# Kernel optimization log

Measured on AMD Instinct MI355X. Metric: run time of the kernel, lower is better.

## Reference

```python
import jax, jax.numpy as jnp
import numpy as np
from jax.scipy.special import logsumexp

B, T, LD, HD, K = 64, 2048, 16, 64, 8
TEMP = 1.0  # annealing=False
LOG2PI = float(np.log(2.0 * np.pi))


def setup_inputs() -> dict:
    key = jax.random.key(0)
    ks = jax.random.split(key, 10)
    return {
        "z": jax.random.normal(ks[0], (B, T, LD), jnp.float32),
        "pi": jax.random.normal(ks[1], (K,), jnp.float32) * 0.5,
        "Q": jax.random.normal(ks[2], (K, K), jnp.float32) * 0.5,
        "init_mean": jax.random.normal(ks[3], (K, LD), jnp.float32),
        # torch init: rand(K,1,1) * eye(LD) * 5  (a scale factor per state)
        "init_cov": jax.random.uniform(ks[4], (K, 1, 1), jnp.float32) * 5.0 * jnp.eye(LD, dtype=jnp.float32)[None],
        "covs": jnp.tile(jnp.eye(LD, dtype=jnp.float32)[None], (K, 1, 1)) + 0.05 * jax.random.normal(ks[5], (K, LD, LD), jnp.float32),
        "W1": jax.random.normal(ks[6], (K, HD, LD), jnp.float32) / np.sqrt(LD),
        "b1": jnp.zeros((K, HD), jnp.float32),
        "W2": jax.random.normal(ks[7], (K, LD, HD), jnp.float32) / np.sqrt(HD),
        "b2": jnp.zeros((K, LD), jnp.float32),
    }


def _chol_terms(C):
    """Sigma = C C^T + 1e-6 I ; return (L^{-1}, 0.5*logdet) per state."""
    dim = C.shape[-1]
    Sigma = C @ jnp.swapaxes(C, -1, -2) + 1e-6 * jnp.eye(dim, dtype=C.dtype)
    L = jnp.linalg.cholesky(Sigma)  # [K,D,D]
    Linv = jax.vmap(lambda l: jax.scipy.linalg.solve_triangular(l, jnp.eye(dim, dtype=C.dtype), lower=True))(L)
    logdet_half = jnp.sum(jnp.log(jnp.diagonal(L, axis1=-2, axis2=-1)), -1)  # [K]
    return Linv, logdet_half


def _mvn_logp(diff, Linv, logdet_half):
    # diff [B,t,K,D], Linv [K,D,D] -> [B,t,K]
    y = jnp.einsum('kde,btke->btkd', Linv, diff)
    maha = jnp.sum(y * y, -1)
    d = diff.shape[-1]
    return -0.5 * maha - logdet_half - 0.5 * d * LOG2PI


def reference(z, pi, Q, init_mean, init_cov, covs, W1, b1, W2, b2):
    # ---- local evidence: log p(z_1|s_1), log p(z_t | z_{t-1}, s_t)  [B,T,K]
    Linv0, ld0 = _chol_terms(init_cov)
    le1 = _mvn_logp(z[:, :1, None, :] - init_mean, Linv0, ld0)  # [B,1,K]
    zp = z[:, :-1]  # [B,T-1,D]
    h = jax.nn.softplus(jnp.einsum('btd,khd->btkh', zp, W1) + b1)  # per-state MLP hidden
    mu = jnp.einsum('btkh,kdh->btkd', h, W2) + b2  # [B,T-1,K,D]
    LinvT, ldT = _chol_terms(covs)
    leT = _mvn_logp(z[:, 1:, None, :] - mu, LinvT, ldT)  # [B,T-1,K]
    le = jnp.concatenate([le1, leT], axis=1)  # [B,T,K]

    # ---- alpha recursion (filtering)
    logpi = jax.nn.log_softmax(pi / TEMP)
    Qlog = jax.nn.log_softmax(Q / TEMP, axis=-1)  # log p(s_t=j | s_{t-1}=i)
    QT = Qlog.T  # [to, from]
    lp0 = le[:, 0] + logpi
    lz0 = logsumexp(lp0, -1)
    la0 = lp0 - lz0[:, None]
    le_rest = jnp.swapaxes(le[:, 1:], 0, 1)  # [T-1,B,K]

    def astep(la_prev, le_t):
        lp = logsumexp(le_t[:, :, None] + QT[None] + la_prev[:, None, :], axis=-1)
        lz = logsumexp(lp, -1)
        la = lp - lz[:, None]
        return la, (la, lz)

    _, (las, lzs) = jax.lax.scan(astep, la0, le_rest)
    log_alpha = jnp.concatenate([la0[:, None], jnp.swapaxes(las, 0, 1)], axis=1)  # [B,T,K]
    log_Z = jnp.concatenate([lz0[:, None], lzs.T], axis=1)  # [B,T]

    # ---- beta recursion (smoothing), reverse scan
    def bstep(lb_next, inp):
        le_t, lz_t = inp
        lb = logsumexp(Qlog[None] + le_t[:, None, :] + lb_next[:, None, :], axis=-1) - lz_t[:, None]
        return lb, lb

    _, lbs = jax.lax.scan(bstep, jnp.zeros((B, K), le.dtype), (le_rest, log_Z[:, 1:].T), reverse=True)
    log_beta = jnp.concatenate([jnp.swapaxes(lbs, 0, 1), jnp.zeros((B, 1, K), le.dtype)], axis=1)

    # ---- posteriors
    gamma = jnp.exp(log_alpha + log_beta)  # [B,T,K]
    paired = jnp.exp(Qlog[None, None] + log_alpha[:, :-1, :, None] + log_beta[:, 1:, None, :] + le[:, 1:, None, :] - log_Z[:, 1:, None, None])  # [B,T-1,K,K]
    return gamma, paired, log_Z
```

## Files before the change

### kernel.cpp

```cpp
#include <hip/hip_runtime.h>

#define B_ 64
#define T_ 2048
#define LD_ 16
#define HD_ 64
#define K_ 8
#define L_ 16
#define C_ 128
#define S_ 16

constexpr int OFF_LE    = 0;
constexpr int OFF_ALPHA = 1048576;
constexpr int OFF_EBAR  = 2097152;
constexpr int OFF_ZT    = OFF_ALPHA;
constexpr int OFF_PBUF  = 3145728;
constexpr int OFF_RLOG  = 3670016;
constexpr int OFF_SBUF  = 3809280;
constexpr int OFF_UBUF  = 3874816;
constexpr int OFF_ULOG  = 3940352;
constexpr int OFF_SAIN  = 3941376;
constexpr int OFF_BENT  = 3949568;
constexpr int OFF_PRM   = 3957760;

constexpr int P_LINV0 = 0;
constexpr int P_LINVT = 2048;
constexpr int P_LD0   = 4096;
constexpr int P_LDT   = 4104;
constexpr int P_LOGPI = 4112;
constexpr int P_QEXP  = 4120;
constexpr int P_QTEXP = 4184;

constexpr int FI_NC2 = 32768;
constexpr int FI_C0I = 32896;

constexpr int OUT_PAIRED = B_*T_*K_;
constexpr int OUT_LOGZ   = OUT_PAIRED + B_*(T_-1)*K_*K_;

template<int CTRL>
__device__ __forceinline__ float dppmov(float x) {
  int xi = __float_as_int(x);
  int r = __builtin_amdgcn_update_dpp(xi, xi, CTRL, 0xF, 0xF, true);
  return __int_as_float(r);
}
__device__ __forceinline__ void allg8(float v, float w[8]) {
  w[0] = v;
  w[1] = dppmov<0xB1>(v);
  w[2] = dppmov<0x4E>(v);
  w[3] = dppmov<0x4E>(w[1]);
  w[7] = dppmov<0x141>(v);
  w[6] = dppmov<0xB1>(w[7]);
  w[5] = dppmov<0x4E>(w[7]);
  w[4] = dppmov<0x4E>(w[6]);
}
template<int V> __device__ __forceinline__ float xorg8(float x);
template<> __device__ __forceinline__ float xorg8<0>(float x) { return x; }
template<> __device__ __forceinline__ float xorg8<1>(float x) { return dppmov<0xB1>(x); }
template<> __device__ __forceinline__ float xorg8<2>(float x) { return dppmov<0x4E>(x); }
template<> __device__ __forceinline__ float xorg8<3>(float x) { return dppmov<0x4E>(dppmov<0xB1>(x)); }
template<> __device__ __forceinline__ float xorg8<4>(float x) { return dppmov<0x4E>(dppmov<0xB1>(dppmov<0x141>(x))); }
template<> __device__ __forceinline__ float xorg8<5>(float x) { return dppmov<0x4E>(dppmov<0x141>(x)); }
template<> __device__ __forceinline__ float xorg8<6>(float x) { return dppmov<0xB1>(dppmov<0x141>(x)); }
template<> __device__ __forceinline__ float xorg8<7>(float x) { return dppmov<0x141>(x); }

__device__ __forceinline__ float bfly_sum8(float x) {
  x += dppmov<0xB1>(x); x += dppmov<0x4E>(x); x += dppmov<0x141>(x); return x;
}
__device__ __forceinline__ float bfly_max8(float x) {
  x = fmaxf(x, dppmov<0xB1>(x)); x = fmaxf(x, dppmov<0x4E>(x)); x = fmaxf(x, dppmov<0x141>(x)); return x;
}
__device__ __forceinline__ float rcpnr(float x) {
  float r0 = __builtin_amdgcn_rcpf(x);
  return r0 * __builtin_fmaf(-x, r0, 2.0f);
}
__device__ __forceinline__ void absg8(float v, float w[8]) {
  int x = __float_as_int(v);
  w[0] = __int_as_float(__builtin_amdgcn_ds_swizzle(x, 0x18));
  w[1] = __int_as_float(__builtin_amdgcn_ds_swizzle(x, 0x38));
  w[2] = __int_as_float(__builtin_amdgcn_ds_swizzle(x, 0x58));
  w[3] = __int_as_float(__builtin_amdgcn_ds_swizzle(x, 0x78));
  w[4] = __int_as_float(__builtin_amdgcn_ds_swizzle(x, 0x98));
  w[5] = __int_as_float(__builtin_amdgcn_ds_swizzle(x, 0xB8));
  w[6] = __int_as_float(__builtin_amdgcn_ds_swizzle(x, 0xD8));
  w[7] = __int_as_float(__builtin_amdgcn_ds_swizzle(x, 0xF8));
}
__device__ __forceinline__ void col2row(const float cl[8], float rv[8]) {
  rv[0] = cl[0];
  rv[1] = xorg8<1>(cl[1]);
  rv[2] = xorg8<2>(cl[2]);
  rv[3] = xorg8<3>(cl[3]);
  rv[4] = xorg8<4>(cl[4]);
  rv[5] = xorg8<5>(cl[5]);
  rv[6] = xorg8<6>(cl[6]);
  rv[7] = xorg8<7>(cl[7]);
}
__device__ __forceinline__ void mmul8(const float a[8], const float m[8], float o[8]) {
  float m8[8][8];
  #pragma unroll
  for (int w = 0; w < 8; w++) allg8(m[w], m8[w]);
  #pragma unroll
  for (int v = 0; v < 8; v++) {
    float acc = 0.f;
    #pragma unroll
    for (int u = 0; u < 8; u++) acc = __builtin_fmaf(a[u], m8[u^v][u], acc);
    o[v] = acc;
  }
}
__device__ __forceinline__ float maxnorm8(float m[8]) {
  float mx = m[0];
  #pragma unroll
  for (int u = 1; u < 8; u++) mx = fmaxf(mx, m[u]);
  mx = bfly_max8(mx);
  float r = rcpnr(mx);
  #pragma unroll
  for (int u = 0; u < 8; u++) m[u] *= r;
  return mx;
}
__device__ __forceinline__ void load_rows(const float* p, float r[8]) {
  const float4* q = (const float4*)p;
  float4 x0 = q[0], x1 = q[1];
  r[0]=x0.x; r[1]=x0.y; r[2]=x0.z; r[3]=x0.w;
  r[4]=x1.x; r[5]=x1.y; r[6]=x1.z; r[7]=x1.w;
}
__device__ __forceinline__ float dotw8(const float r[8], const float w[8]) {
  return ((r[0]*w[0]+r[1]*w[1]) + (r[2]*w[2]+r[3]*w[3]))
       + ((r[4]*w[4]+r[5]*w[5]) + (r[6]*w[6]+r[7]*w[7]));
}

typedef __attribute__((ext_vector_type(4))) float f32x4;
typedef __attribute__((ext_vector_type(8))) short bf16x8;

__device__ __forceinline__ unsigned ph(float a, float b) {
  return (__float_as_uint(a) >> 16) | (__float_as_uint(b) & 0xFFFF0000u);
}
__device__ __forceinline__ float hif(float a) {
  return __uint_as_float(__float_as_uint(a) & 0xFFFF0000u);
}
__device__ __forceinline__ bf16x8 u2f(uint4 u) {
  return __builtin_bit_cast(bf16x8, u);
}
__device__ __forceinline__ uint4 mkfrag_u4(float4 v) {
  unsigned ux = __float_as_uint(v.x), uy = __float_as_uint(v.y);
  unsigned uz = __float_as_uint(v.z), uw = __float_as_uint(v.w);
  unsigned h01 = (ux >> 16) | (uy & 0xFFFF0000u);
  unsigned h23 = (uz >> 16) | (uw & 0xFFFF0000u);
  float lx = v.x - __uint_as_float(ux & 0xFFFF0000u);
  float ly = v.y - __uint_as_float(uy & 0xFFFF0000u);
  float lz = v.z - __uint_as_float(uz & 0xFFFF0000u);
  float lw = v.w - __uint_as_float(uw & 0xFFFF0000u);
  unsigned l01 = ph(lx, ly);
  unsigned l23 = ph(lz, lw);
  return make_uint4(h01, h23, l01, l23);
}
__device__ __forceinline__ f32x4 MF(bf16x8 a, bf16x8 b, f32x4 c) {
  return __builtin_amdgcn_mfma_f32_16x16x32_bf16(a, b, c, 0, 0, 0);
}

__global__ __launch_bounds__(64) void prep_kernel(
    const float* __restrict__ pi, const float* __restrict__ Q,
    const float* __restrict__ init_cov, const float* __restrict__ covs,
    float* __restrict__ prm)
{
  int tid = threadIdx.x;
  int blk = blockIdx.x;
  if (blk < 16) {
    int k = blk & 7;
    const float* C = (blk < 8 ? init_cov : covs) + k*256;
    float* outL  = prm + (blk < 8 ? P_LINV0 : P_LINVT) + k*256;
    float* outld = prm + (blk < 8 ? P_LD0   : P_LDT)   + k;
    __shared__ float S[16][17], L[16][17], X[16][17];
    for (int e = tid; e < 256; e += 64) {
      int r = e >> 4, c = e & 15;
      float s = (r == c) ? 1e-6f : 0.f;
      for (int l = 0; l < 16; l++) s += C[r*16+l] * C[c*16+l];
      S[r][c] = s;
    }
    __syncthreads();
    for (int j = 0; j < 16; j++) {
      if (tid == 0) L[j][j] = sqrtf(S[j][j]);
      __syncthreads();
      if (tid > j && tid < 16) L[tid][j] = S[tid][j] / L[j][j];
      __syncthreads();
      if (tid > j && tid < 16) {
        float ltj = L[tid][j];
        for (int c = j+1; c <= tid; c++) S[tid][c] -= ltj * L[c][j];
      }
      __syncthreads();
    }
    if (tid < 16) {
      int c = tid;
      for (int r = 0; r < 16; r++) {
        float v;
        if (r < c) v = 0.f;
        else {
          v = (r == c) ? 1.f : 0.f;
          for (int s2 = c; s2 < r; s2++) v -= L[r][s2] * X[s2][c];
          v /= L[r][r];
        }
        X[r][c] = v;
      }
    }
    __syncthreads();
    for (int e = tid; e < 256; e += 64) outL[e] = X[e>>4][e&15];
    if (tid == 0) {
      float ld = 0.f;
      for (int j = 0; j < 16; j++) ld += logf(L[j][j]);
      *outld = ld;
    }
  } else {
    if (tid < 8) {
      int row = tid;
      float q[8], mx = -1e30f;
      for (int j = 0; j < 8; j++) { q[j] = Q[row*8+j]; mx = fmaxf(mx, q[j]); }
      float s = 0.f;
      for (int j = 0; j < 8; j++) s += __expf(q[j]-mx);
      float ls = logf(s);
      for (int j = 0; j < 8; j++) {
        float e = __expf(q[j]-mx-ls);
        prm[P_QEXP  + row*8 + j] = e;
        prm[P_QTEXP + j*8 + row] = e;
      }
    } else if (tid == 8) {
      float p[8], mx = -1e30f;
      for (int j = 0; j < 8; j++) { p[j] = pi[j]; mx = fmaxf(mx, p[j]); }
      float s = 0.f;
      for (int j = 0; j < 8; j++) s += __expf(p[j]-mx);
      float ls = logf(s);
      for (int j = 0; j < 8; j++) prm[P_LOGPI+j] = p[j]-mx-ls;
    }
  }
}

__global__ __launch_bounds__(64) void prep2_kernel(
    const float* __restrict__ W1, const float* __restrict__ W2,
    const float* __restrict__ b2, const float* __restrict__ init_mean,
    const float* __restrict__ prm, float* __restrict__ frag)
{
  int k = blockIdx.x, tid = threadIdx.x;
  __shared__ float Ls[16][16], L0s[16][16], G[16][64];
  for (int e = tid; e < 256; e += 64) {
    Ls[e>>4][e&15]  = prm[P_LINVT + k*256 + e];
    L0s[e>>4][e&15] = prm[P_LINV0 + k*256 + e];
  }
  __syncthreads();
  for (int idx = tid; idx < 1024; idx += 64) {
    int d = idx >> 6, hh = idx & 63;
    float s = 0.f;
    for (int e = 0; e < 16; e++) s += Ls[d][e] * W2[k*1024 + e*64 + hh];
    G[d][hh] = -s;
  }
  __syncthreads();
  int d = tid & 15, q = tid >> 4;
  uint4* F4 = (uint4*)frag;
  for (int kc = 0; kc < 2; kc++) {
    float v[8], lo[8];
    for (int j = 0; j < 8; j++) {
      int hh = 32*kc + 16*(j>>2) + 4*q + (j&3);
      v[j] = G[d][hh];
      lo[j] = v[j] - hif(v[j]);
    }
    F4[6144 + ((k*2+kc)*4+q)*16 + d] =
        make_uint4(ph(v[0],v[1]), ph(v[2],v[3]), ph(v[4],v[5]), ph(v[6],v[7]));
    F4[7168 + ((k*2+kc)*4+q)*16 + d] =
        make_uint4(ph(lo[0],lo[1]), ph(lo[2],lo[3]), ph(lo[4],lo[5]), ph(lo[6],lo[7]));
  }
  for (int mt = 0; mt < 4; mt++) {
    int hh = 16*mt + d;
    float v[4], lo[4];
    for (int j = 0; j < 4; j++) { v[j] = W1[k*1024 + hh*16 + 4*q + j]; lo[j] = v[j] - hif(v[j]); }
    unsigned x = ph(v[0],v[1]), y = ph(v[2],v[3]);
    F4[((k*4+mt)*4+q)*16 + d]        = make_uint4(x, y, x, y);
    F4[2048 + ((k*4+mt)*4+q)*16 + d] = make_uint4(ph(lo[0],lo[1]), ph(lo[2],lo[3]), 0u, 0u);
  }
  {
    float v[4], lo[4];
    for (int j = 0; j < 4; j++) { v[j] = Ls[d][4*q+j]; lo[j] = v[j] - hif(v[j]); }
    unsigned x = ph(v[0],v[1]), y = ph(v[2],v[3]);
    F4[4096 + (k*4+q)*16 + d] = make_uint4(x, y, x, y);
    F4[4608 + (k*4+q)*16 + d] = make_uint4(ph(lo[0],lo[1]), ph(lo[2],lo[3]), 0u, 0u);
    for (int j = 0; j < 4; j++) { v[j] = L0s[d][4*q+j]; lo[j] = v[j] - hif(v[j]); }
    x = ph(v[0],v[1]); y = ph(v[2],v[3]);
    F4[5120 + (k*4+q)*16 + d] = make_uint4(x, y, x, y);
    F4[5632 + (k*4+q)*16 + d] = make_uint4(ph(lo[0],lo[1]), ph(lo[2],lo[3]), 0u, 0u);
  }
  if (q == 0) {
    float s2 = 0.f, s0 = 0.f;
    for (int e = 0; e < 16; e++) {
      s2 += Ls[d][e]  * b2[k*16+e];
      s0 += L0s[d][e] * init_mean[k*16+e];
    }
    frag[FI_NC2 + k*16 + d] = -s2;
    frag[FI_C0I + k*16 + d] = -s0;
  }
}

__global__ __launch_bounds__(256) void ztr_kernel(
    const float* __restrict__ z, uint4* __restrict__ zf)
{
  int tid = blockIdx.x*256 + threadIdx.x;
  int t = tid >> 6, b = tid & 63;
  const float4* src = (const float4*)(z + (b*T_ + t)*LD_);
  #pragma unroll
  for (int q = 0; q < 4; q++)
    zf[(t*4 + q)*64 + b] = mkfrag_u4(src[q]);
}

__global__ __launch_bounds__(256) void emisB_kernel(
    const uint4* __restrict__ zf, const float* __restrict__ b1,
    const float* __restrict__ frag, const float* __restrict__ prm,
    float* __restrict__ lebuf)
{
  int lane = threadIdx.x & 63;
  int wid = __builtin_amdgcn_readfirstlane(blockIdx.x*4 + (threadIdx.x >> 6));
  int bblk = wid & 3;
  int tch  = (wid >> 2) & 255;
  int k    = wid >> 10;
  int c = lane & 15, q = lane >> 4;
  int b = bblk*16 + c;
  const uint4* F4 = (const uint4*)frag;

  bf16x8 w1a1[4], w1a2[4];
  #pragma unroll
  for (int mt = 0; mt < 4; mt++) {
    w1a1[mt] = u2f(F4[((k*4+mt)*4+q)*16 + c]);
    w1a2[mt] = u2f(F4[2048 + ((k*4+mt)*4+q)*16 + c]);
  }
  bf16x8 lva1 = u2f(F4[4096 + (k*4+q)*16 + c]);
  bf16x8 lva2 = u2f(F4[4608 + (k*4+q)*16 + c]);
  bf16x8 gahi[2], galo[2];
  #pragma unroll
  for (int kc = 0; kc < 2; kc++) {
    gahi[kc] = u2f(F4[6144 + ((k*2+kc)*4+q)*16 + c]);
    galo[kc] = u2f(F4[7168 + ((k*2+kc)*4+q)*16 + c]);
  }
  float b1iv[16];
  #pragma unroll
  for (int i = 0; i < 16; i++)
    b1iv[i] = b1[k*64 + (i>>2)*16 + 4*q + (i&3)];
  float nc2[4];
  #pragma unroll
  for (int r = 0; r < 4; r++) nc2[r] = frag[FI_NC2 + k*16 + 4*q + r];
  float lconst = -prm[P_LDT + k] - 14.70301653f;

  int t0 = tch*8;
  bf16x8 zp;
  int ttstart;
  if (tch == 0) {
    bf16x8 zc0 = u2f(zf[q*64 + b]);
    bf16x8 l0a1 = u2f(F4[5120 + (k*4+q)*16 + c]);
    bf16x8 l0a2 = u2f(F4[5632 + (k*4+q)*16 + c]);
    f32x4 acc;
    acc[0] = frag[FI_C0I + k*16 + 4*q + 0];
    acc[1] = frag[FI_C0I + k*16 + 4*q + 1];
    acc[2] = frag[FI_C0I + k*16 + 4*q + 2];
    acc[3] = frag[FI_C0I + k*16 + 4*q + 3];
    acc = MF(l0a1, zc0, acc);
    acc = MF(l0a2, zc0, acc);
    float m2 = (acc[0]*acc[0] + acc[1]*acc[1]) + (acc[2]*acc[2] + acc[3]*acc[3]);
    m2 += __shfl_xor(m2, 16);
    m2 += __shfl_xor(m2, 32);
    float le = -0.5f*m2 - prm[P_LD0+k] - 14.70301653f + prm[P_LOGPI+k];
    if (q == 0) lebuf[k*64 + b] = le;
    zp = zc0;
    ttstart = 1;
  } else {
    zp = u2f(zf[((t0-1)*4 + q)*64 + b]);
    ttstart = 0;
  }

  uint4 zvu = zf[((t0+ttstart)*4 + q)*64 + b];
  #pragma unroll 1
  for (int tt = ttstart; tt < 8; tt++) {
    int t = t0 + tt;
    uint4 zvn = zvu;
    if (tt < 7) zvn = zf[((t+1)*4 + q)*64 + b];
    bf16x8 zc = u2f(zvu);
    f32x4 a1[4];
    #pragma unroll
    for (int mt = 0; mt < 4; mt++) {
      f32x4 ai;
      ai[0] = b1iv[mt*4+0]; ai[1] = b1iv[mt*4+1];
      ai[2] = b1iv[mt*4+2]; ai[3] = b1iv[mt*4+3];
      ai = MF(w1a1[mt], zp, ai);
      a1[mt] = MF(w1a2[mt], zp, ai);
    }
    float hv[16];
    #pragma unroll
    for (int i = 0; i < 16; i++) {
      float a = a1[i>>2][i&3];
      hv[i] = __logf(1.f + __expf(a));
    }
    bf16x8 hhi[2], hlo[2];
    #pragma unroll
    for (int kc = 0; kc < 2; kc++) {
      const float* hp = hv + 8*kc;
      hhi[kc] = u2f(make_uint4(ph(hp[0],hp[1]), ph(hp[2],hp[3]),
                               ph(hp[4],hp[5]), ph(hp[6],hp[7])));
      float l0 = hp[0]-hif(hp[0]), l1 = hp[1]-hif(hp[1]);
      float l2 = hp[2]-hif(hp[2]), l3 = hp[3]-hif(hp[3]);
      float l4 = hp[4]-hif(hp[4]), l5 = hp[5]-hif(hp[5]);
      float l6 = hp[6]-hif(hp[6]), l7 = hp[7]-hif(hp[7]);
      hlo[kc] = u2f(make_uint4(ph(l0,l1), ph(l2,l3), ph(l4,l5), ph(l6,l7)));
    }
    f32x4 acc;
    acc[0] = nc2[0]; acc[1] = nc2[1]; acc[2] = nc2[2]; acc[3] = nc2[3];
    acc = MF(lva1, zc, acc);
    acc = MF(lva2, zc, acc);
    #pragma unroll
    for (int kc = 0; kc < 2; kc++) {
      acc = MF(gahi[kc], hhi[kc], acc);
      acc = MF(galo[kc], hhi[kc], acc);
      acc = MF(gahi[kc], hlo[kc], acc);
    }
    float m2 = (acc[0]*acc[0] + acc[1]*acc[1]) + (acc[2]*acc[2] + acc[3]*acc[3]);
    m2 += __shfl_xor(m2, 16);
    m2 += __shfl_xor(m2, 32);
    float le = -0.5f*m2 + lconst;
    if (q == 0) lebuf[t*512 + k*64 + b] = le;
    zp = zc;
    zvu = zvn;
  }
}

__global__ __launch_bounds__(256) void fwdA_kernel(
    const float* __restrict__ lebuf, const float* __restrict__ prm,
    float* __restrict__ pbuf, float* __restrict__ sbuf)
{
  int lane64 = threadIdx.x & 63;
  int iu = threadIdx.x >> 6;
  int unit = blockIdx.x*4 + iu;
  int b = unit & 63, s = unit >> 6;
  int u = lane64 >> 3, j = lane64 & 7;
  int c = 8*s + u;
  float qtv[64];
  #pragma unroll
  for (int x = 0; x < 8; x++)
    #pragma unroll
    for (int v = 0; v < 8; v++)
      qtv[x*8+v] = prm[P_QTEXP + (j^x)*8 + (j^v)];
  float lev[16];
  #pragma unroll
  for (int x = 0; x < 16; x++) lev[x] = lebuf[(c*L_+x)*512 + j*64 + b];
  float pl[8];
  if (c == 0) {
    float m = bfly_max8(lev[0]);
    float e = __expf(lev[0]-m);
    allg8(e, pl);
  } else {
    float m = bfly_max8(lev[0]);
    float e = __expf(lev[0]-m);
    float e8[8]; allg8(e, e8);
    float np[8];
    #pragma unroll
    for (int x = 0; x < 8; x++) np[x] = e8[x] * qtv[x*8];
    float mx = np[0];
    #pragma unroll
    for (int x = 1; x < 8; x++) mx = fmaxf(mx, np[x]);
    mx = bfly_max8(mx);
    float r = rcpnr(mx);
    #pragma unroll
    for (int x = 0; x < 8; x++) pl[x] = np[x] * r;
  }
  #pragma unroll
  for (int sx = 1; sx < 16; sx++) {
    float m = bfly_max8(lev[sx]);
    float e = __expf(lev[sx]-m);
    float e8[8]; allg8(e, e8);
    float np[8];
    #pragma unroll
    for (int x = 0; x < 8; x++) {
      float acc = 0.f;
      #pragma unroll
      for (int v = 0; v < 8; v++) acc = __builtin_fmaf(qtv[x*8+v], pl[v], acc);
      np[x] = e8[x] * acc;
    }
    float mx = np[0];
    #pragma unroll
    for (int x = 1; x < 8; x++) mx = fmaxf(mx, np[x]);
    mx = bfly_max8(mx);
    float r = rcpnr(mx);
    #pragma unroll
    for (int x = 0; x < 8; x++) pl[x] = np[x] * r;
  }
  float rv[8]; col2row(pl, rv);
  float4* dst = (float4*)(pbuf + (c*64 + b)*64 + j*8);
  dst[0] = make_float4(rv[0], rv[1], rv[2], rv[3]);
  dst[1] = make_float4(rv[4], rv[5], rv[6], rv[7]);
  __shared__ float M[4][8][64];
  #pragma unroll
  for (int v = 0; v < 8; v++) M[iu][u][j*8+v] = rv[v];
  __syncthreads();
  if (u == 0) {
    float m[8];
    #pragma unroll
    for (int v = 0; v < 8; v++) m[v] = M[iu][0][j*8+v];
    for (int cc = 1; cc < 8; cc++) {
      float a[8];
      #pragma unroll
      for (int v = 0; v < 8; v++) a[v] = M[iu][cc][j*8+v];
      float nm[8];
      mmul8(a, m, nm);
      maxnorm8(nm);
      #pragma unroll
      for (int v = 0; v < 8; v++) m[v] = nm[v];
    }
    float4* d2 = (float4*)(sbuf + (s*64 + b)*64 + j*8);
    d2[0] = make_float4(m[0], m[1], m[2], m[3]);
    d2[1] = make_float4(m[4], m[5], m[6], m[7]);
  }
}

__global__ __launch_bounds__(512) void fwdP2b_kernel(
    const float* __restrict__ sbuf, float* __restrict__ sain)
{
  int lane = threadIdx.x;
  int b = lane >> 3, i = lane & 7;
  const float4* base = (const float4*)sbuf;
  float4 c0 = base[(0*64+b)*16 + i*2], c1 = base[(0*64+b)*16 + i*2 + 1];
  float a = 0.125f;
  for (int s = 0; s < 16; s++) {
    int s2 = (s < 15) ? s+1 : 15;
    float4 n0 = base[(s2*64+b)*16 + i*2], n1 = base[(s2*64+b)*16 + i*2 + 1];
    float aw[8]; allg8(a, aw);
    float sm = ((c0.x*aw[0] + c0.y*aw[1]) + (c0.z*aw[2] + c0.w*aw[3]))
             + ((c1.x*aw[4] + c1.y*aw[5]) + (c1.z*aw[6] + c1.w*aw[7]));
    float tot = bfly_sum8(sm);
    float an = sm * rcpnr(tot);
    if (s < 15) { a = an; sain[(s+1)*512 + b*8 + i] = a; }
    c0 = n0; c1 = n1;
  }
}

__global__ __launch_bounds__(256) void fwdB_kernel(
    const float* __restrict__ lebuf, const float* __restrict__ prm,
    const float* __restrict__ sain, float* pbuf,
    float* __restrict__ alpha, float* __restrict__ ebar,
    float* __restrict__ rlog, float* __restrict__ ubuf,
    float* __restrict__ ulog, float* __restrict__ out)
{
  int lane64 = threadIdx.x & 63;
  int iu = threadIdx.x >> 6;
  int unit = blockIdx.x*4 + iu;
  int b = unit & 63, s = unit >> 6;
  int u = lane64 >> 3, i = lane64 & 7;
  int c = 8*s + u;
  int off = b*8 + i;
  __shared__ float Als[4][8];
  __shared__ float Mh[4][8][64];
  __shared__ float Lh[4][8];
  float pr[8];
  load_rows(pbuf + (c*64 + b)*64 + i*8, pr);
  float lev[16];
  #pragma unroll
  for (int x = 0; x < 16; x++) lev[x] = lebuf[(c*L_+x)*512 + i*64 + b];
  float av_in = 0.f;
  if (u == 0) av_in = (s == 0) ? 0.125f : sain[s*512 + off];
  for (int r = 0; r < 7; r++) {
    if (u == r) {
      if (r > 0) av_in = Als[iu][i];
      float aw[8]; allg8(av_in, aw);
      float sm = dotw8(pr, aw);
      float tot = bfly_sum8(sm);
      Als[iu][i] = sm * rcpnr(tot);
    }
    __syncthreads();
  }
  if (u == 7) av_in = Als[iu][i];
  float q[8];
  #pragma unroll
  for (int x = 0; x < 8; x++) q[x] = prm[P_QTEXP + i*8 + (i^x)];
  float* logZ = out + OUT_LOGZ + b*T_;
  float eb_loc[16];
  float a;
  if (c == 0) {
    float m0 = bfly_max8(lev[0]);
    float e0x = __expf(lev[0]-m0);
    float ct = bfly_sum8(e0x);
    float rr = rcpnr(ct);
    a = e0x * rr;
    alpha[off] = a;
    eb_loc[0] = a;
    ebar[off] = a;
    if (i == 0) logZ[0] = m0 + __logf(ct);
  } else {
    a = av_in;
    int t = c*L_;
    float m = bfly_max8(lev[0]);
    float e = __expf(lev[0]-m);
    float w[8]; allg8(a, w);
    float dot = dotw8(q, w);
    float p = e * dot;
    float ct = bfly_sum8(p);
    float rr = rcpnr(ct);
    a = p * rr;
    alpha[t*512 + off] = a;
    float eb = e * rr;
    eb_loc[0] = eb;
    ebar[t*512 + off] = eb;
    if (i == 0) logZ[t] = m + __logf(ct);
  }
  #pragma unroll
  for (int x = 1; x < 16; x++) {
    int t = c*L_ + x;
    float m = bfly_max8(lev[x]);
    float e = __expf(lev[x]-m);
    float w[8]; allg8(a, w);
    float dot = dotw8(q, w);
    float p = e * dot;
    float ct = bfly_sum8(p);
    float rr = rcpnr(ct);
    a = p * rr;
    alpha[t*512 + off] = a;
    float eb = e * rr;
    eb_loc[x] = eb;
    ebar[t*512 + off] = eb;
    if (i == 0) logZ[t] = m + __logf(ct);
  }
  float qv[64];
  #pragma unroll
  for (int x = 0; x < 8; x++)
    #pragma unroll
    for (int v = 0; v < 8; v++)
      qv[x*8+v] = prm[P_QEXP + (i^x)*8 + (i^v)];
  float rl8[8];
  #pragma unroll
  for (int x = 0; x < 8; x++) rl8[x] = (x == 0) ? 1.f : 0.f;
  float lsc = 0.f;
  #pragma unroll
  for (int sx = 15; sx >= 1; sx--) {
    float e8[8]; allg8(eb_loc[sx], e8);
    float nr[8];
    #pragma unroll
    for (int x = 0; x < 8; x++) {
      float acc = 0.f;
      #pragma unroll
      for (int v = 0; v < 8; v++) acc = __builtin_fmaf(qv[x*8+v], e8[v]*rl8[v], acc);
      nr[x] = acc;
    }
    float mx = nr[0];
    #pragma unroll
    for (int x = 1; x < 8; x++) mx = fmaxf(mx, nr[x]);
    mx = bfly_max8(mx);
    float r = rcpnr(mx);
    #pragma unroll
    for (int x = 0; x < 8; x++) rl8[x] = nr[x] * r;
    lsc += __logf(mx);
  }
  float rv[8]; col2row(rl8, rv);
  float4* dstR = (float4*)(pbuf + (c*64 + b)*64 + i*8);
  dstR[0] = make_float4(rv[0], rv[1], rv[2], rv[3]);
  dstR[1] = make_float4(rv[4], rv[5], rv[6], rv[7]);
  if (i == 0) rlog[c*64 + b] = lsc;
  float qr[8];
  #pragma unroll
  for (int x = 0; x < 8; x++) qr[x] = prm[P_QEXP + i*8 + (i^x)];
  float d8[8];
  #pragma unroll
  for (int v = 0; v < 8; v++) d8[v] = eb_loc[0] * rv[v];
  float h8[8];
  mmul8(qr, d8, h8);
  float ls = lsc + __logf(maxnorm8(h8));
  #pragma unroll
  for (int v = 0; v < 8; v++) Mh[iu][u][i*8+v] = h8[v];
  if (i == 0) Lh[iu][u] = ls;
  __syncthreads();
  if (u == 0) {
    float m[8];
    #pragma unroll
    for (int v = 0; v < 8; v++) m[v] = Mh[iu][7][i*8+v];
    float lsum = Lh[iu][7];
    for (int cc = 6; cc >= 0; cc--) {
      float aa[8];
      #pragma unroll
      for (int v = 0; v < 8; v++) aa[v] = Mh[iu][cc][i*8+v];
      float t8[8];
      mmul8(aa, m, t8);
      lsum += Lh[iu][cc] + __logf(maxnorm8(t8));
      #pragma unroll
      for (int v = 0; v < 8; v++) m[v] = t8[v];
    }
    float4* d2 = (float4*)(ubuf + (s*64 + b)*64 + i*8);
    d2[0] = make_float4(m[0], m[1], m[2], m[3]);
    d2[1] = make_float4(m[4], m[5], m[6], m[7]);
    if (i == 0) ulog[s*64 + b] = lsum;
  }
}

__global__ __launch_bounds__(512) void bwdP2b_kernel(
    const float* __restrict__ ubuf, const float* __restrict__ ulog,
    float* __restrict__ bent)
{
  int lane = threadIdx.x;
  int b = lane >> 3, i = lane & 7;
  bent[15*512 + b*8 + i] = 1.f;
  const float4* base = (const float4*)ubuf;
  float sh = 1.f, sig = 0.f;
  float4 c0 = base[(15*64+b)*16 + i*2], c1 = base[(15*64+b)*16 + i*2 + 1];
  float cu = ulog[15*64 + b];
  for (int s = 15; s >= 1; s--) {
    int s2 = (s > 1) ? s-1 : 1;
    float4 n0 = base[(s2*64+b)*16 + i*2], n1 = base[(s2*64+b)*16 + i*2 + 1];
    float nu = ulog[s2*64 + b];
    float sw[8]; allg8(sh, sw);
    float y = ((c0.x*sw[0] + c0.y*sw[1]) + (c0.z*sw[2] + c0.w*sw[3]))
            + ((c1.x*sw[4] + c1.y*sw[5]) + (c1.z*sw[6] + c1.w*sw[7]));
    float mx = bfly_max8(y);
    sh = y * rcpnr(mx);
    sig += cu + __logf(mx);
    bent[(s-1)*512 + b*8 + i] = sh * __expf(sig);
    c0 = n0; c1 = n1; cu = nu;
  }
}

__global__ __launch_bounds__(256) void bwdC_kernel(
    const float* __restrict__ alpha, const float* __restrict__ ebar,
    const float* __restrict__ rbuf, const float* __restrict__ rlog,
    const float* __restrict__ prm, const float* __restrict__ bent,
    float* __restrict__ out)
{
  int lane64 = threadIdx.x & 63;
  int iu = threadIdx.x >> 6;
  int unit = blockIdx.x*4 + iu;
  int b = unit & 63, s = unit >> 6;
  int u = lane64 >> 3, i = lane64 & 7;
  int c = 8*s + u;
  int off = b*8 + i;
  float qr[8], qa[8];
  #pragma unroll
  for (int x = 0; x < 8; x++) qr[x] = prm[P_QEXP + i*8 + (i^x)];
  #pragma unroll
  for (int v = 0; v < 8; v++) qa[v] = prm[P_QEXP + i*8 + v];
  float r8[8];
  load_rows(rbuf + (c*64 + b)*64 + i*8, r8);
  float e0 = ebar[(c*L_)*512 + off];
  float erl = __expf(rlog[c*64 + b]);
  float av[16], ev[16];
  #pragma unroll
  for (int x = 0; x < 16; x++) av[x] = alpha[(c*L_+x)*512 + off];
  #pragma unroll
  for (int x = 1; x < 16; x++) ev[x] = ebar[(c*L_+x)*512 + off];
  float avm1 = (c > 0) ? alpha[(c*L_-1)*512 + off] : 0.f;
  __shared__ float Bls[4][8];
  float bt = 0.f, y = 0.f, nbv = 0.f;
  for (int r = 7; r >= 0; r--) {
    if (u == r) {
      bt = (r == 7) ? bent[s*512 + off] : Bls[iu][i];
      float bw[8]; allg8(bt, bw);
      y = dotw8(r8, bw) * erl;
      float ey = e0 * y;
      float w[8]; allg8(ey, w);
      nbv = 0.f;
      #pragma unroll
      for (int v = 0; v < 8; v++) nbv = __builtin_fmaf(qr[v], w[v], nbv);
      if (r > 0) Bls[iu][i] = nbv;
    }
    __syncthreads();
  }
  float* po = out + OUT_PAIRED + b*((T_-1)*64);
  float* go = out + b*(T_*K_);
  float bb = bt;
  if (c == 127) go[2047*8 + i] = av[15];
  #pragma unroll
  for (int x = 15; x >= 1; x--) {
    float eya[8]; absg8(ev[x]*bb, eya);
    float term[8];
    #pragma unroll
    for (int v = 0; v < 8; v++) term[v] = qa[v]*eya[v];
    float nb = ((term[0]+term[1]) + (term[2]+term[3]))
             + ((term[4]+term[5]) + (term[6]+term[7]));
    int t = c*L_ + x - 1;
    float am = av[x-1];
    float4* pd = (float4*)(po + t*64 + i*8);
    pd[0] = make_float4(am*term[0], am*term[1], am*term[2], am*term[3]);
    pd[1] = make_float4(am*term[4], am*term[5], am*term[6], am*term[7]);
    go[t*8 + i] = am*nb;
    bb = nb;
  }
  if (c > 0) {
    float eya[8]; absg8(e0*y, eya);
    int t = c*L_ - 1;
    float4* pd = (float4*)(po + t*64 + i*8);
    pd[0] = make_float4(avm1*qa[0]*eya[0], avm1*qa[1]*eya[1],
                        avm1*qa[2]*eya[2], avm1*qa[3]*eya[3]);
    pd[1] = make_float4(avm1*qa[4]*eya[4], avm1*qa[5]*eya[5],
                        avm1*qa[6]*eya[6], avm1*qa[7]*eya[7]);
    go[t*8 + i] = avm1 * nbv;
  }
}

extern "C" void kernel_launch(void* const* d_in, const int* in_sizes, int n_in,
                              void* d_out, int out_size, void* d_ws, size_t ws_size,
                              hipStream_t stream) {
  const float* z         = (const float*)d_in[0];
  const float* pi        = (const float*)d_in[1];
  const float* Q         = (const float*)d_in[2];
  const float* init_mean = (const float*)d_in[3];
  const float* init_cov  = (const float*)d_in[4];
  const float* covs      = (const float*)d_in[5];
  const float* W1        = (const float*)d_in[6];
  const float* b1        = (const float*)d_in[7];
  const float* W2        = (const float*)d_in[8];
  const float* b2        = (const float*)d_in[9];
  float* out = (float*)d_out;
  float* ws  = (float*)d_ws;

  prep_kernel<<<17, 64, 0, stream>>>(pi, Q, init_cov, covs, ws + OFF_PRM);
  prep2_kernel<<<8, 64, 0, stream>>>(W1, W2, b2, init_mean, ws + OFF_PRM,
                                     ws + OFF_UBUF);
  ztr_kernel<<<512, 256, 0, stream>>>(z, (uint4*)(ws + OFF_ZT));
  emisB_kernel<<<2048, 256, 0, stream>>>((const uint4*)(ws + OFF_ZT), b1,
                                         ws + OFF_UBUF, ws + OFF_PRM,
                                         ws + OFF_LE);
  fwdA_kernel<<<256, 256, 0, stream>>>(ws + OFF_LE, ws + OFF_PRM,
                                       ws + OFF_PBUF, ws + OFF_SBUF);
  fwdP2b_kernel<<<1, 512, 0, stream>>>(ws + OFF_SBUF, ws + OFF_SAIN);
  fwdB_kernel<<<256, 256, 0, stream>>>(ws + OFF_LE, ws + OFF_PRM, ws + OFF_SAIN,
                                       ws + OFF_PBUF, ws + OFF_ALPHA,
                                       ws + OFF_EBAR, ws + OFF_RLOG,
                                       ws + OFF_UBUF, ws + OFF_ULOG, out);
  bwdP2b_kernel<<<1, 512, 0, stream>>>(ws + OFF_UBUF, ws + OFF_ULOG, ws + OFF_BENT);
  bwdC_kernel<<<256, 256, 0, stream>>>(ws + OFF_ALPHA, ws + OFF_EBAR,
                                       ws + OFF_PBUF, ws + OFF_RLOG,
                                       ws + OFF_PRM, ws + OFF_BENT, out);
}
```

Before: 283.9 us.

## Halve HMM chunk length, drop ebar buffer, compute Q softmax per block

Reduces the per-chunk time length of the chunked forward/backward scan from 16 to 8, doubling the number of chunks and blocks. This shortens the serial work per thread and the register footprint, at the cost of longer sequential cross-chunk passes (32 steps instead of 16). The ebar intermediate is no longer written to global memory. The backward kernel instead recomputes it from the log-evidence and logZ, trading extra exp work for less memory traffic. The softmax of Q is computed in shared memory inside each block rather than read from a precomputed parameter buffer.

Result: faster. 234.1 us (-17.5%).

```diff
diff --git a/kernel.cpp b/kernel.cpp
--- a/kernel.cpp
+++ b/kernel.cpp
@@ -5,30 +5,28 @@
 #define LD_ 16
 #define HD_ 64
 #define K_ 8
-#define L_ 16
-#define C_ 128
-#define S_ 16
+#define L_ 8
+#define C_ 256
+#define S_ 32
 
 constexpr int OFF_LE    = 0;
 constexpr int OFF_ALPHA = 1048576;
-constexpr int OFF_EBAR  = 2097152;
 constexpr int OFF_ZT    = OFF_ALPHA;
-constexpr int OFF_PBUF  = 3145728;
-constexpr int OFF_RLOG  = 3670016;
-constexpr int OFF_SBUF  = 3809280;
-constexpr int OFF_UBUF  = 3874816;
-constexpr int OFF_ULOG  = 3940352;
-constexpr int OFF_SAIN  = 3941376;
-constexpr int OFF_BENT  = 3949568;
-constexpr int OFF_PRM   = 3957760;
+constexpr int OFF_SBUF  = 2097152;
+constexpr int OFF_UBUF  = 2228224;
+constexpr int OFF_RLOG  = 2359296;
+constexpr int OFF_ULOG  = 2375680;
+constexpr int OFF_SAIN  = 2377728;
+constexpr int OFF_BENT  = 2394112;
+constexpr int OFF_PBUF  = 2410496;
+constexpr int OFF_PRML  = 3459072;
+constexpr int OFF_FRAG  = 3463680;
 
 constexpr int P_LINV0 = 0;
 constexpr int P_LINVT = 2048;
 constexpr int P_LD0   = 4096;
 constexpr int P_LDT   = 4104;
 constexpr int P_LOGPI = 4112;
-constexpr int P_QEXP  = 4120;
-constexpr int P_QTEXP = 4184;
 
 constexpr int FI_NC2 = 32768;
 constexpr int FI_C0I = 32896;
@@ -125,6 +123,20 @@
   return ((r[0]*w[0]+r[1]*w[1]) + (r[2]*w[2]+r[3]*w[3]))
        + ((r[4]*w[4]+r[5]*w[5]) + (r[6]*w[6]+r[7]*w[7]));
 }
+__device__ __forceinline__ void fill_Qe(const float* __restrict__ Qm, float* Qe) {
+  if (threadIdx.x < 8) {
+    int r = threadIdx.x;
+    float qq[8], mx = -1e30f;
+    #pragma unroll
+    for (int c2 = 0; c2 < 8; c2++) { qq[c2] = Qm[r*8+c2]; mx = fmaxf(mx, qq[c2]); }
+    float s = 0.f;
+    #pragma unroll
+    for (int c2 = 0; c2 < 8; c2++) s += __expf(qq[c2]-mx);
+    float ls = __logf(s);
+    #pragma unroll
+    for (int c2 = 0; c2 < 8; c2++) Qe[r*8+c2] = __expf(qq[c2]-mx-ls);
+  }
+}
 
 typedef __attribute__((ext_vector_type(4))) float f32x4;
 typedef __attribute__((ext_vector_type(8))) short bf16x8;
@@ -147,9 +159,7 @@
   float ly = v.y - __uint_as_float(uy & 0xFFFF0000u);
   float lz = v.z - __uint_as_float(uz & 0xFFFF0000u);
   float lw = v.w - __uint_as_float(uw & 0xFFFF0000u);
-  unsigned l01 = ph(lx, ly);
-  unsigned l23 = ph(lz, lw);
-  return make_uint4(h01, h23, l01, l23);
+  return make_uint4(h01, h23, ph(lx,ly), ph(lz,lw));
 }
 __device__ __forceinline__ f32x4 MF(bf16x8 a, bf16x8 b, f32x4 c) {
   return __builtin_amdgcn_mfma_f32_16x16x32_bf16(a, b, c, 0, 0, 0);
@@ -207,19 +217,7 @@
       *outld = ld;
     }
   } else {
-    if (tid < 8) {
-      int row = tid;
-      float q[8], mx = -1e30f;
-      for (int j = 0; j < 8; j++) { q[j] = Q[row*8+j]; mx = fmaxf(mx, q[j]); }
-      float s = 0.f;
-      for (int j = 0; j < 8; j++) s += __expf(q[j]-mx);
-      float ls = logf(s);
-      for (int j = 0; j < 8; j++) {
-        float e = __expf(q[j]-mx-ls);
-        prm[P_QEXP  + row*8 + j] = e;
-        prm[P_QTEXP + j*8 + row] = e;
-      }
-    } else if (tid == 8) {
+    if (tid == 0) {
       float p[8], mx = -1e30f;
       for (int j = 0; j < 8; j++) { p[j] = pi[j]; mx = fmaxf(mx, p[j]); }
       float s = 0.f;
@@ -422,24 +420,28 @@
 }
 
 __global__ __launch_bounds__(256) void fwdA_kernel(
-    const float* __restrict__ lebuf, const float* __restrict__ prm,
+    const float* __restrict__ lebuf, const float* __restrict__ Qm,
     float* __restrict__ pbuf, float* __restrict__ sbuf)
 {
+  __shared__ float Qe[64];
+  __shared__ float M[4][8][64];
+  fill_Qe(Qm, Qe);
   int lane64 = threadIdx.x & 63;
   int iu = threadIdx.x >> 6;
   int unit = blockIdx.x*4 + iu;
   int b = unit & 63, s = unit >> 6;
   int u = lane64 >> 3, j = lane64 & 7;
   int c = 8*s + u;
+  float lev[8];
+  #pragma unroll
+  for (int x = 0; x < 8; x++) lev[x] = lebuf[(c*L_+x)*512 + j*64 + b];
+  __syncthreads();
   float qtv[64];
   #pragma unroll
   for (int x = 0; x < 8; x++)
     #pragma unroll
     for (int v = 0; v < 8; v++)
-      qtv[x*8+v] = prm[P_QTEXP + (j^x)*8 + (j^v)];
-  float lev[16];
-  #pragma unroll
-  for (int x = 0; x < 16; x++) lev[x] = lebuf[(c*L_+x)*512 + j*64 + b];
+      qtv[x*8+v] = Qe[(j^v)*8 + (j^x)];
   float pl[8];
   if (c == 0) {
     float m = bfly_max8(lev[0]);
@@ -461,7 +463,7 @@
     for (int x = 0; x < 8; x++) pl[x] = np[x] * r;
   }
   #pragma unroll
-  for (int sx = 1; sx < 16; sx++) {
+  for (int sx = 1; sx < 8; sx++) {
     float m = bfly_max8(lev[sx]);
     float e = __expf(lev[sx]-m);
     float e8[8]; allg8(e, e8);
@@ -485,7 +487,6 @@
   float4* dst = (float4*)(pbuf + (c*64 + b)*64 + j*8);
   dst[0] = make_float4(rv[0], rv[1], rv[2], rv[3]);
   dst[1] = make_float4(rv[4], rv[5], rv[6], rv[7]);
-  __shared__ float M[4][8][64];
   #pragma unroll
   for (int v = 0; v < 8; v++) M[iu][u][j*8+v] = rv[v];
   __syncthreads();
@@ -517,26 +518,31 @@
   const float4* base = (const float4*)sbuf;
   float4 c0 = base[(0*64+b)*16 + i*2], c1 = base[(0*64+b)*16 + i*2 + 1];
   float a = 0.125f;
-  for (int s = 0; s < 16; s++) {
-    int s2 = (s < 15) ? s+1 : 15;
+  for (int s = 0; s < S_; s++) {
+    int s2 = (s < S_-1) ? s+1 : S_-1;
     float4 n0 = base[(s2*64+b)*16 + i*2], n1 = base[(s2*64+b)*16 + i*2 + 1];
     float aw[8]; allg8(a, aw);
     float sm = ((c0.x*aw[0] + c0.y*aw[1]) + (c0.z*aw[2] + c0.w*aw[3]))
              + ((c1.x*aw[4] + c1.y*aw[5]) + (c1.z*aw[6] + c1.w*aw[7]));
     float tot = bfly_sum8(sm);
     float an = sm * rcpnr(tot);
-    if (s < 15) { a = an; sain[(s+1)*512 + b*8 + i] = a; }
+    if (s < S_-1) { a = an; sain[(s+1)*512 + b*8 + i] = a; }
     c0 = n0; c1 = n1;
   }
 }
 
 __global__ __launch_bounds__(256) void fwdB_kernel(
-    const float* __restrict__ lebuf, const float* __restrict__ prm,
+    const float* __restrict__ lebuf, const float* __restrict__ Qm,
     const float* __restrict__ sain, float* pbuf,
-    float* __restrict__ alpha, float* __restrict__ ebar,
-    float* __restrict__ rlog, float* __restrict__ ubuf,
-    float* __restrict__ ulog, float* __restrict__ out)
+    float* __restrict__ alpha, float* __restrict__ rlog,
+    float* __restrict__ ubuf, float* __restrict__ ulog,
+    float* __restrict__ out)
 {
+  __shared__ float Qe[64];
+  __shared__ float Als[4][8];
+  __shared__ float Mh[4][8][64];
+  __shared__ float Lh[4][8];
+  fill_Qe(Qm, Qe);
   int lane64 = threadIdx.x & 63;
   int iu = threadIdx.x >> 6;
   int unit = blockIdx.x*4 + iu;
@@ -544,14 +550,15 @@
   int u = lane64 >> 3, i = lane64 & 7;
   int c = 8*s + u;
   int off = b*8 + i;
-  __shared__ float Als[4][8];
-  __shared__ float Mh[4][8][64];
-  __shared__ float Lh[4][8];
   float pr[8];
   load_rows(pbuf + (c*64 + b)*64 + i*8, pr);
-  float lev[16];
-  #pragma unroll
-  for (int x = 0; x < 16; x++) lev[x] = lebuf[(c*L_+x)*512 + i*64 + b];
+  float lev[8];
+  #pragma unroll
+  for (int x = 0; x < 8; x++) lev[x] = lebuf[(c*L_+x)*512 + i*64 + b];
+  __syncthreads();
+  float q[8];
+  #pragma unroll
+  for (int x = 0; x < 8; x++) q[x] = Qe[(i^x)*8 + i];
   float av_in = 0.f;
   if (u == 0) av_in = (s == 0) ? 0.125f : sain[s*512 + off];
   for (int r = 0; r < 7; r++) {
@@ -565,11 +572,8 @@
     __syncthreads();
   }
   if (u == 7) av_in = Als[iu][i];
-  float q[8];
-  #pragma unroll
-  for (int x = 0; x < 8; x++) q[x] = prm[P_QTEXP + i*8 + (i^x)];
   float* logZ = out + OUT_LOGZ + b*T_;
-  float eb_loc[16];
+  float eb_loc[8];
   float a;
   if (c == 0) {
     float m0 = bfly_max8(lev[0]);
@@ -579,7 +583,6 @@
     a = e0x * rr;
     alpha[off] = a;
     eb_loc[0] = a;
-    ebar[off] = a;
     if (i == 0) logZ[0] = m0 + __logf(ct);
   } else {
     a = av_in;
@@ -593,13 +596,11 @@
     float rr = rcpnr(ct);
     a = p * rr;
     alpha[t*512 + off] = a;
-    float eb = e * rr;
-    eb_loc[0] = eb;
-    ebar[t*512 + off] = eb;
+    eb_loc[0] = e * rr;
     if (i == 0) logZ[t] = m + __logf(ct);
   }
   #pragma unroll
-  for (int x = 1; x < 16; x++) {
+  for (int x = 1; x < 8; x++) {
     int t = c*L_ + x;
     float m = bfly_max8(lev[x]);
     float e = __expf(lev[x]-m);
@@ -610,9 +611,7 @@
     float rr = rcpnr(ct);
     a = p * rr;
     alpha[t*512 + off] = a;
-    float eb = e * rr;
-    eb_loc[x] = eb;
-    ebar[t*512 + off] = eb;
+    eb_loc[x] = e * rr;
     if (i == 0) logZ[t] = m + __logf(ct);
   }
   float qv[64];
@@ -620,13 +619,13 @@
   for (int x = 0; x < 8; x++)
     #pragma unroll
     for (int v = 0; v < 8; v++)
-      qv[x*8+v] = prm[P_QEXP + (i^x)*8 + (i^v)];
+      qv[x*8+v] = Qe[(i^x)*8 + (i^v)];
   float rl8[8];
   #pragma unroll
   for (int x = 0; x < 8; x++) rl8[x] = (x == 0) ? 1.f : 0.f;
   float lsc = 0.f;
   #pragma unroll
-  for (int sx = 15; sx >= 1; sx--) {
+  for (int sx = 7; sx >= 1; sx--) {
     float e8[8]; allg8(eb_loc[sx], e8);
     float nr[8];
     #pragma unroll
@@ -652,7 +651,7 @@
   if (i == 0) rlog[c*64 + b] = lsc;
   float qr[8];
   #pragma unroll
-  for (int x = 0; x < 8; x++) qr[x] = prm[P_QEXP + i*8 + (i^x)];
+  for (int x = 0; x < 8; x++) qr[x] = Qe[i*8 + (i^x)];
   float d8[8];
   #pragma unroll
   for (int v = 0; v < 8; v++) d8[v] = eb_loc[0] * rv[v];
@@ -691,12 +690,12 @@
 {
   int lane = threadIdx.x;
   int b = lane >> 3, i = lane & 7;
-  bent[15*512 + b*8 + i] = 1.f;
+  bent[(S_-1)*512 + b*8 + i] = 1.f;
   const float4* base = (const float4*)ubuf;
   float sh = 1.f, sig = 0.f;
-  float4 c0 = base[(15*64+b)*16 + i*2], c1 = base[(15*64+b)*16 + i*2 + 1];
-  float cu = ulog[15*64 + b];
-  for (int s = 15; s >= 1; s--) {
+  float4 c0 = base[((S_-1)*64+b)*16 + i*2], c1 = base[((S_-1)*64+b)*16 + i*2 + 1];
+  float cu = ulog[(S_-1)*64 + b];
+  for (int s = S_-1; s >= 1; s--) {
     int s2 = (s > 1) ? s-1 : 1;
     float4 n0 = base[(s2*64+b)*16 + i*2], n1 = base[(s2*64+b)*16 + i*2 + 1];
     float nu = ulog[s2*64 + b];
@@ -712,11 +711,14 @@
 }
 
 __global__ __launch_bounds__(256) void bwdC_kernel(
-    const float* __restrict__ alpha, const float* __restrict__ ebar,
+    const float* __restrict__ alpha, const float* __restrict__ lebuf,
     const float* __restrict__ rbuf, const float* __restrict__ rlog,
-    const float* __restrict__ prm, const float* __restrict__ bent,
+    const float* __restrict__ Qm, const float* __restrict__ bent,
     float* __restrict__ out)
 {
+  __shared__ float Qe[64];
+  __shared__ float Bls[4][8];
+  fill_Qe(Qm, Qe);
   int lane64 = threadIdx.x & 63;
   int iu = threadIdx.x >> 6;
   int unit = blockIdx.x*4 + iu;
@@ -724,22 +726,30 @@
   int u = lane64 >> 3, i = lane64 & 7;
   int c = 8*s + u;
   int off = b*8 + i;
-  float qr[8], qa[8];
-  #pragma unroll
-  for (int x = 0; x < 8; x++) qr[x] = prm[P_QEXP + i*8 + (i^x)];
-  #pragma unroll
-  for (int v = 0; v < 8; v++) qa[v] = prm[P_QEXP + i*8 + v];
   float r8[8];
   load_rows(rbuf + (c*64 + b)*64 + i*8, r8);
-  float e0 = ebar[(c*L_)*512 + off];
   float erl = __expf(rlog[c*64 + b]);
-  float av[16], ev[16];
-  #pragma unroll
-  for (int x = 0; x < 16; x++) av[x] = alpha[(c*L_+x)*512 + off];
-  #pragma unroll
-  for (int x = 1; x < 16; x++) ev[x] = ebar[(c*L_+x)*512 + off];
+  float av[8], lev[8];
+  #pragma unroll
+  for (int x = 0; x < 8; x++) av[x] = alpha[(c*L_+x)*512 + off];
+  #pragma unroll
+  for (int x = 0; x < 8; x++) lev[x] = lebuf[(c*L_+x)*512 + i*64 + b];
+  const float* lzp = out + OUT_LOGZ + b*T_ + c*L_;
+  float4 lz0 = *(const float4*)lzp;
+  float4 lz1 = *(const float4*)(lzp + 4);
+  float ev[8];
+  ev[0] = __expf(lev[0]-lz0.x); ev[1] = __expf(lev[1]-lz0.y);
+  ev[2] = __expf(lev[2]-lz0.z); ev[3] = __expf(lev[3]-lz0.w);
+  ev[4] = __expf(lev[4]-lz1.x); ev[5] = __expf(lev[5]-lz1.y);
+  ev[6] = __expf(lev[6]-lz1.z); ev[7] = __expf(lev[7]-lz1.w);
+  float e0 = ev[0];
   float avm1 = (c > 0) ? alpha[(c*L_-1)*512 + off] : 0.f;
-  __shared__ float Bls[4][8];
+  __syncthreads();
+  float qr[8], qa[8];
+  #pragma unroll
+  for (int x = 0; x < 8; x++) qr[x] = Qe[i*8 + (i^x)];
+  #pragma unroll
+  for (int v = 0; v < 8; v++) qa[v] = Qe[i*8 + v];
   float bt = 0.f, y = 0.f, nbv = 0.f;
   for (int r = 7; r >= 0; r--) {
     if (u == r) {
@@ -758,9 +768,9 @@
   float* po = out + OUT_PAIRED + b*((T_-1)*64);
   float* go = out + b*(T_*K_);
   float bb = bt;
-  if (c == 127) go[2047*8 + i] = av[15];
-  #pragma unroll
-  for (int x = 15; x >= 1; x--) {
+  if (c == C_-1) go[2047*8 + i] = av[7];
+  #pragma unroll
+  for (int x = 7; x >= 1; x--) {
     float eya[8]; absg8(ev[x]*bb, eya);
     float term[8];
     #pragma unroll
@@ -803,22 +813,23 @@
   float* out = (float*)d_out;
   float* ws  = (float*)d_ws;
 
-  prep_kernel<<<17, 64, 0, stream>>>(pi, Q, init_cov, covs, ws + OFF_PRM);
-  prep2_kernel<<<8, 64, 0, stream>>>(W1, W2, b2, init_mean, ws + OFF_PRM,
-                                     ws + OFF_UBUF);
+  prep_kernel<<<17, 64, 0, stream>>>(pi, Q, init_cov, covs, ws + OFF_PRML);
+  prep2_kernel<<<8, 64, 0, stream>>>(W1, W2, b2, init_mean, ws + OFF_PRML,
+                                     ws + OFF_FRAG);
   ztr_kernel<<<512, 256, 0, stream>>>(z, (uint4*)(ws + OFF_ZT));
   emisB_kernel<<<2048, 256, 0, stream>>>((const uint4*)(ws + OFF_ZT), b1,
-                                         ws + OFF_UBUF, ws + OFF_PRM,
+                                         ws + OFF_FRAG, ws + OFF_PRML,
                                          ws + OFF_LE);
-  fwdA_kernel<<<256, 256, 0, stream>>>(ws + OFF_LE, ws + OFF_PRM,
-                                       ws + OFF_PBUF, ws + OFF_SBUF);
+  fwdA_kernel<<<512, 256, 0, stream>>>(ws + OFF_LE, Q, ws + OFF_PBUF,
+                                       ws + OFF_SBUF);
   fwdP2b_kernel<<<1, 512, 0, stream>>>(ws + OFF_SBUF, ws + OFF_SAIN);
-  fwdB_kernel<<<256, 256, 0, stream>>>(ws + OFF_LE, ws + OFF_PRM, ws + OFF_SAIN,
+  fwdB_kernel<<<512, 256, 0, stream>>>(ws + OFF_LE, Q, ws + OFF_SAIN,
                                        ws + OFF_PBUF, ws + OFF_ALPHA,
-                                       ws + OFF_EBAR, ws + OFF_RLOG,
-                                       ws + OFF_UBUF, ws + OFF_ULOG, out);
-  bwdP2b_kernel<<<1, 512, 0, stream>>>(ws + OFF_UBUF, ws + OFF_ULOG, ws + OFF_BENT);
-  bwdC_kernel<<<256, 256, 0, stream>>>(ws + OFF_ALPHA, ws + OFF_EBAR,
-                                       ws + OFF_PBUF, ws + OFF_RLOG,
-                                       ws + OFF_PRM, ws + OFF_BENT, out);
-}
+                                       ws + OFF_RLOG, ws + OFF_UBUF,
+                                       ws + OFF_ULOG, out);
+  bwdP2b_kernel<<<1, 512, 0, stream>>>(ws + OFF_UBUF, ws + OFF_ULOG,
+                                       ws + OFF_BENT);
+  bwdC_kernel<<<512, 256, 0, stream>>>(ws + OFF_ALPHA, ws + OFF_LE,
+                                       ws + OFF_PBUF, ws + OFF_RLOG, Q,
+                                       ws + OFF_BENT, out);
+}
```
